# Kernel tuning notes

Hardware: AMD Instinct MI355X
Metric: run time of the kernel (lower is better)

## Reference

```python
import jax, jax.numpy as jnp
import numpy as np

EPS = 1e-5  # BatchNorm1d default eps


def _knn_idx(coords, k):
    # squared pairwise distances via gram trick (monotone in cdist, same topk order)
    sq = jnp.sum(coords * coords, axis=-1)                     # [B,N]
    d2 = sq[:, :, None] + sq[:, None, :] - 2.0 * jnp.einsum('bnd,bmd->bnm', coords, coords)
    _, idx = jax.lax.top_k(-d2, k)                             # smallest distances
    return idx                                                  # [B,N,k]


def _shared_mlp(x, W, b, gamma, beta):
    # Linear -> BatchNorm1d (training-mode batch stats over B,N per channel) -> ReLU
    y = x @ W + b                                              # [B,N,C]
    m = jnp.mean(y, axis=(0, 1))
    v = jnp.var(y, axis=(0, 1))                                # biased, as torch BN
    y = (y - m) / jnp.sqrt(v + EPS) * gamma + beta
    return jax.nn.relu(y)


def setup_inputs() -> dict:
    key = jax.random.key(0)
    ks = jax.random.split(key, 16)
    B, N, in_ch, out_ch, k = 4, 8192, 64, 128, 16
    mid = out_ch // 2
    s = 0.05
    inp = {
        'coords': jax.random.normal(ks[0], (B, N, 3), jnp.float32),
        'feats': jax.random.normal(ks[1], (B, N, in_ch), jnp.float32),
        'k': k,
        'W1': jax.random.normal(ks[2], (in_ch, mid), jnp.float32) * s,
        'b1': jnp.zeros((mid,), jnp.float32),
        'g1': jnp.ones((mid,), jnp.float32),
        'be1': jnp.zeros((mid,), jnp.float32),
        'Wa': jax.random.normal(ks[3], (mid, mid), jnp.float32) * s,
        'ba': jnp.zeros((mid,), jnp.float32),
        'ga': jnp.ones((mid,), jnp.float32),
        'bea': jnp.zeros((mid,), jnp.float32),
        'W2': jax.random.normal(ks[4], (mid, out_ch), jnp.float32) * s,
        'b2': jnp.zeros((out_ch,), jnp.float32),
        'g2': jnp.ones((out_ch,), jnp.float32),
        'be2': jnp.zeros((out_ch,), jnp.float32),
    }
    return inp


def reference(coords, feats, k, W1, b1, g1, be1, Wa, ba, ga, bea, W2, b2, g2, be2):
    B, N, _ = coords.shape
    idx = _knn_idx(coords, k)                                  # [B,N,k]
    # gather neighbor features: feats[b, idx[b,n,j]]
    neighbors = feats[jnp.arange(B)[:, None, None], idx]       # [B,N,k,C_in]
    agg = _shared_mlp(neighbors.mean(axis=2), W1, b1, g1, be1) # [B,N,mid]
    attn = jax.nn.sigmoid(_shared_mlp(agg, Wa, ba, ga, bea))
    fused = agg * attn + agg
    return _shared_mlp(fused, W2, b2, g2, be2)                 # [B,N,out_ch]
```

## Files before the change

### kernel.cpp

```cpp
#include <hip/hip_runtime.h>
#include <hip/hip_bf16.h>
#include <hip/hip_fp16.h>
#include <math.h>

#define B_ 4
#define N_ 8192
#define K_ 16
#define BN_ (B_ * N_)
#define EPS_ 1e-5f

#define S_ 8
#define TPB (S_ * 64)
#define QPB 64
#define MCAND (N_ / S_)
#define DEPTH 16

#define NBLK 512
#define ROWS 64

__global__ __launch_bounds__(256) void pack_coords(const float* __restrict__ coords,
                                                   float4* __restrict__ out) {
    int i = blockIdx.x * 256 + threadIdx.x;
    if (i >= BN_) return;
    out[i] = make_float4(coords[3 * i], coords[3 * i + 1], coords[3 * i + 2], 0.0f);
}

__global__ __launch_bounds__(256) void feats2h(const float* __restrict__ in,
                                               __half* __restrict__ outh) {
    int i = blockIdx.x * 256 + threadIdx.x;
    const float4* p = (const float4*)(in + (size_t)i * 8);
    float4 a = p[0], b = p[1];
    __half2 h0; h0.x = __float2half_rn(a.x); h0.y = __float2half_rn(a.y);
    __half2 h1; h1.x = __float2half_rn(a.z); h1.y = __float2half_rn(a.w);
    __half2 h2; h2.x = __float2half_rn(b.x); h2.y = __float2half_rn(b.y);
    __half2 h3; h3.x = __float2half_rn(b.z); h3.y = __float2half_rn(b.w);
    uint4 o;
    o.x = *(unsigned*)&h0; o.y = *(unsigned*)&h1; o.z = *(unsigned*)&h2; o.w = *(unsigned*)&h3;
    ((uint4*)outh)[i] = o;
}

__global__ __launch_bounds__(512) void knn_kernel(const float4* __restrict__ coords4,
                                                  int* __restrict__ idxOut) {
    __shared__ float2 bufp[DEPTH][TPB];
    __shared__ float thr2d[S_][64];

    const int bpb = N_ / QPB;
    int b = blockIdx.x / bpb;
    int qbase = (blockIdx.x % bpb) * QPB;
    int t = threadIdx.x;
    int lane = t & 63;
    int w = __builtin_amdgcn_readfirstlane(t >> 6);
    int q = qbase + lane;

    thr2d[t >> 6][lane] = 3.4e38f;
    __syncthreads();

    const float4* cb = coords4 + (size_t)b * N_;
    float4 qc = cb[q];
    float qx = qc.x, qy = qc.y, qz = qc.z;

    float key[K_];
    int   id[K_];
#pragma unroll
    for (int j = 0; j < K_; j++) { key[j] = 3.4e38f; id[j] = -1; }

    int cnt = 0;
    float bound = 3.4e38f;
    float lim = 3.4e38f;

    auto flush = [&]() {
        for (int j = 0; j < cnt; ++j) {
            float2 e = bufp[j][t];
            float d2 = e.x;
            int   m  = __float_as_int(e.y);
            if (d2 < key[K_ - 1]) {
#pragma unroll
                for (int jj = K_ - 1; jj > 0; --jj) {
                    bool up = d2 < key[jj - 1];
                    float ik = fminf(d2, key[jj]);
                    int   ii = (d2 < key[jj]) ? m : id[jj];
                    key[jj] = up ? key[jj - 1] : ik;
                    id[jj]  = up ? id[jj - 1]  : ii;
                }
                if (d2 < key[0]) { key[0] = d2; id[0] = m; }
            }
        }
        cnt = 0;
    };

    auto proc = [&](float4 c, int m) {
        float dx = qx - c.x, dy = qy - c.y, dz = qz - c.z;
        float d2 = dx * dx;
        d2 = fmaf(dy, dy, d2);
        d2 = fmaf(dz, dz, d2);
        if (d2 < lim) {
            bufp[cnt][t] = make_float2(d2, __int_as_float(m));
            cnt++;
        }
    };

    const int base = w * MCAND;
    for (int i = 0; i < MCAND; i += 8) {
        float4 c0 = cb[base + i + 0];
        float4 c1 = cb[base + i + 1];
        float4 c2 = cb[base + i + 2];
        float4 c3 = cb[base + i + 3];
        float4 c4 = cb[base + i + 4];
        float4 c5 = cb[base + i + 5];
        float4 c6 = cb[base + i + 6];
        float4 c7 = cb[base + i + 7];
        proc(c0, base + i + 0);
        proc(c1, base + i + 1);
        proc(c2, base + i + 2);
        proc(c3, base + i + 3);
        proc(c4, base + i + 4);
        proc(c5, base + i + 5);
        proc(c6, base + i + 6);
        proc(c7, base + i + 7);
        if (__any(cnt >= DEPTH - 7)) {
            flush();
            lim = fminf(key[K_ - 1], bound);
        }
        if ((i & 56) == 56) {
            thr2d[w][lane] = key[K_ - 1];
            float m0 = fminf(thr2d[0][lane], thr2d[1][lane]);
            float m1 = fminf(thr2d[2][lane], thr2d[3][lane]);
            float m2 = fminf(thr2d[4][lane], thr2d[5][lane]);
            float m3 = fminf(thr2d[6][lane], thr2d[7][lane]);
            bound = fminf(fminf(m0, m1), fminf(m2, m3));
            lim = fminf(key[K_ - 1], bound);
        }
    }
    flush();

#pragma unroll
    for (int j = 0; j < K_; j++) bufp[j][t] = make_float2(key[j], __int_as_float(id[j]));

    int* op = idxOut + ((size_t)b * N_ + q) * K_;
    for (int step = 1; step < S_; step <<= 1) {
        bool active = (w & (2 * step - 1)) == 0;
        float md[K_];
        int   mi[K_];
        __syncthreads();
        if (active) {
            int pa = t, pb = t + step * 64;
            int ia = 0, ib = 0;
#pragma unroll
            for (int r = 0; r < K_; ++r) {
                float2 ea = bufp[ia][pa];
                float2 eb = bufp[ib][pb];
                bool sel = ea.x <= eb.x;
                md[r] = sel ? ea.x : eb.x;
                mi[r] = __float_as_int(sel ? ea.y : eb.y);
                ia += sel ? 1 : 0;
                ib += sel ? 0 : 1;
            }
        }
        __syncthreads();
        if (active) {
            if (step == S_ / 2) {
#pragma unroll
                for (int r = 0; r < K_; ++r) op[r] = mi[r];
            } else {
#pragma unroll
                for (int r = 0; r < K_; ++r) bufp[r][t] = make_float2(md[r], __int_as_float(mi[r]));
            }
        }
    }
}

__global__ __launch_bounds__(512) void g1_kernel(const __half* __restrict__ fh,
                                                 const int* __restrict__ idx,
                                                 const float* __restrict__ W1,
                                                 const float* __restrict__ b1,
                                                 float* __restrict__ Y1,
                                                 float* __restrict__ part1) {
    __shared__ float buf[ROWS][65];
    int t = threadIdx.x;
    int rl = t & 63;
    int h2 = __builtin_amdgcn_readfirstlane(t >> 6);
    int vbid = ((blockIdx.x & 7) << 6) + (blockIdx.x >> 3);
    int row = vbid * ROWS + rl;
    int bb = row >> 13;

    const __half* fb = fh + ((size_t)bb << 13) * 64;
    const int* ip = idx + (size_t)row * K_;

    float xh[8];
#pragma unroll
    for (int j = 0; j < 8; j++) xh[j] = 0.0f;
#pragma unroll
    for (int j = 0; j < K_; j++) {
        uint4 a = *(const uint4*)(fb + (((size_t)ip[j]) << 6) + h2 * 8);
        __half2* hp = (__half2*)&a;
#pragma unroll
        for (int p = 0; p < 4; p++) {
            float2 f = __half22float2(hp[p]);
            xh[2 * p] += f.x;
            xh[2 * p + 1] += f.y;
        }
    }
#pragma unroll
    for (int j = 0; j < 8; j++) buf[rl][h2 * 8 + j] = xh[j] * (1.0f / 16.0f);
    __syncthreads();

    float acc[8];
#pragma unroll
    for (int j = 0; j < 8; j++) acc[j] = b1[h2 * 8 + j];
#pragma unroll 1
    for (int c0 = 0; c0 < 64; c0 += 16) {
        float xr[16];
#pragma unroll
        for (int j = 0; j < 16; j++) xr[j] = buf[rl][c0 + j];
#pragma unroll
        for (int cc = 0; cc < 16; cc++) {
            float xv = xr[cc];
            const float* wr = W1 + (c0 + cc) * 64 + h2 * 8;
#pragma unroll
            for (int j = 0; j < 8; j++) acc[j] = fmaf(xv, wr[j], acc[j]);
        }
    }
    float2* yp = (float2*)(Y1 + (size_t)row * 64 + h2 * 8);
#pragma unroll
    for (int f = 0; f < 4; f++) yp[f] = make_float2(acc[2 * f], acc[2 * f + 1]);
    __syncthreads();
#pragma unroll
    for (int j = 0; j < 8; j++) buf[rl][h2 * 8 + j] = acc[j];
    __syncthreads();
    if (t < 128) {
        int c = t & 63;
        float s = 0.0f;
        if (t < 64) { for (int r = 0; r < ROWS; ++r) s += buf[r][c]; }
        else        { for (int r = 0; r < ROWS; ++r) { float v = buf[r][c]; s = fmaf(v, v, s); } }
        part1[blockIdx.x * 128 + t] = s;
    }
}

__device__ __forceinline__ void reduce_stats64(const float* __restrict__ part,
                                               const float* __restrict__ gma,
                                               const float* __restrict__ bta,
                                               float* red4, float* scs, float* shs) {
    int t = threadIdx.x;
    {
        int c = t & 127;
        int q = t >> 7;
        float s = 0.0f;
#pragma unroll 8
        for (int g = q * 128; g < q * 128 + 128; ++g) s += part[(size_t)g * 128 + c];
        red4[t] = s;
    }
    __syncthreads();
    if (t < 128) red4[t] = red4[t] + red4[t + 128] + red4[t + 256] + red4[t + 384];
    __syncthreads();
    if (t < 64) {
        float mean = red4[t] * (1.0f / BN_);
        float var = red4[t + 64] * (1.0f / BN_) - mean * mean;
        float rstd = rsqrtf(var + EPS_);
        float scl = rstd * gma[t];
        scs[t] = scl;
        shs[t] = bta[t] - mean * scl;
    }
    __syncthreads();
}

__global__ __launch_bounds__(512) void m2_kernel(const float* __restrict__ Y1,
                                                 const float* __restrict__ Wa,
                                                 const float* __restrict__ ba,
                                                 const float* __restrict__ g1,
                                                 const float* __restrict__ be1,
                                                 const float* __restrict__ part1,
                                                 float* __restrict__ X1,
                                                 float* __restrict__ Y2,
                                                 float* __restrict__ part2) {
    __shared__ float buf[ROWS][65];
    __shared__ float red4[512];
    __shared__ float scs[64], shs[64];
    int t = threadIdx.x;
    int rl = t & 63;
    int h2 = __builtin_amdgcn_readfirstlane(t >> 6);
    int row = blockIdx.x * ROWS + rl;

    reduce_stats64(part1, g1, be1, red4, scs, shs);

    const float2* y1p = (const float2*)(Y1 + (size_t)row * 64 + h2 * 8);
    float2* x1p = (float2*)(X1 + (size_t)row * 64 + h2 * 8);
#pragma unroll
    for (int f = 0; f < 4; f++) {
        float2 v = y1p[f];
        int c0 = h2 * 8 + 2 * f;
        float a = fmaxf(0.0f, fmaf(v.x, scs[c0], shs[c0]));
        float b = fmaxf(0.0f, fmaf(v.y, scs[c0 + 1], shs[c0 + 1]));
        x1p[f] = make_float2(a, b);
        buf[rl][c0] = a;
        buf[rl][c0 + 1] = b;
    }
    __syncthreads();

    float acc[8];
#pragma unroll
    for (int j = 0; j < 8; j++) acc[j] = ba[h2 * 8 + j];
#pragma unroll 1
    for (int c0 = 0; c0 < 64; c0 += 16) {
        float xr[16];
#pragma unroll
        for (int j = 0; j < 16; j++) xr[j] = buf[rl][c0 + j];
#pragma unroll
        for (int cc = 0; cc < 16; cc++) {
            float xv = xr[cc];
            const float* wr = Wa + (c0 + cc) * 64 + h2 * 8;
#pragma unroll
            for (int j = 0; j < 8; j++) acc[j] = fmaf(xv, wr[j], acc[j]);
        }
    }
    float2* y2p = (float2*)(Y2 + (size_t)row * 64 + h2 * 8);
#pragma unroll
    for (int f = 0; f < 4; f++) y2p[f] = make_float2(acc[2 * f], acc[2 * f + 1]);
    __syncthreads();
#pragma unroll
    for (int j = 0; j < 8; j++) buf[rl][h2 * 8 + j] = acc[j];
    __syncthreads();
    if (t < 128) {
        int c = t & 63;
        float s = 0.0f;
        if (t < 64) { for (int r = 0; r < ROWS; ++r) s += buf[r][c]; }
        else        { for (int r = 0; r < ROWS; ++r) { float v = buf[r][c]; s = fmaf(v, v, s); } }
        part2[blockIdx.x * 128 + t] = s;
    }
}

__global__ __launch_bounds__(512) void m3_kernel(const float* __restrict__ Y2,
                                                 const float* __restrict__ X1,
                                                 const float* __restrict__ W2,
                                                 const float* __restrict__ b2,
                                                 const float* __restrict__ ga,
                                                 const float* __restrict__ bea,
                                                 const float* __restrict__ part2,
                                                 float* __restrict__ Y3,
                                                 float* __restrict__ part3) {
    __shared__ float buf[ROWS][65];
    __shared__ float red4[512];
    __shared__ float scs[64], shs[64];
    int t = threadIdx.x;
    int rl = t & 63;
    int h2 = __builtin_amdgcn_readfirstlane(t >> 6);
    int row = blockIdx.x * ROWS + rl;

    reduce_stats64(part2, ga, bea, red4, scs, shs);

    const float2* y2p = (const float2*)(Y2 + (size_t)row * 64 + h2 * 8);
    const float2* x1p = (const float2*)(X1 + (size_t)row * 64 + h2 * 8);
#pragma unroll
    for (int f = 0; f < 4; f++) {
        float2 v = y2p[f];
        float2 u = x1p[f];
        int c0 = h2 * 8 + 2 * f;
        float t0 = fmaxf(0.0f, fmaf(v.x, scs[c0], shs[c0]));
        float t1 = fmaxf(0.0f, fmaf(v.y, scs[c0 + 1], shs[c0 + 1]));
        float a0 = 1.0f / (1.0f + __expf(-t0));
        float a1 = 1.0f / (1.0f + __expf(-t1));
        buf[rl][c0] = u.x * (1.0f + a0);
        buf[rl][c0 + 1] = u.y * (1.0f + a1);
    }
    __syncthreads();

    float acc16[16];
#pragma unroll
    for (int j = 0; j < 16; j++) acc16[j] = b2[h2 * 16 + j];
#pragma unroll 1
    for (int c0 = 0; c0 < 64; c0 += 16) {
        float xr[16];
#pragma unroll
        for (int j = 0; j < 16; j++) xr[j] = buf[rl][c0 + j];
#pragma unroll
        for (int cc = 0; cc < 16; cc++) {
            float xv = xr[cc];
            const float* wr = W2 + (c0 + cc) * 128 + h2 * 16;
#pragma unroll
            for (int j = 0; j < 16; j++) acc16[j] = fmaf(xv, wr[j], acc16[j]);
        }
    }
    float4* yp = (float4*)(Y3 + (size_t)row * 128 + h2 * 16);
#pragma unroll
    for (int f = 0; f < 4; f++)
        yp[f] = make_float4(acc16[4 * f], acc16[4 * f + 1], acc16[4 * f + 2], acc16[4 * f + 3]);

    __syncthreads();
    if (h2 < 4) {
#pragma unroll
        for (int j = 0; j < 16; j++) buf[rl][h2 * 16 + j] = acc16[j];
    }
    __syncthreads();
    if (t < 128) {
        int c = t & 63;
        float s = 0.0f;
        if (t < 64) { for (int r = 0; r < ROWS; ++r) s += buf[r][c]; }
        else        { for (int r = 0; r < ROWS; ++r) { float v = buf[r][c]; s = fmaf(v, v, s); } }
        part3[blockIdx.x * 256 + t] = s;
    }
    __syncthreads();
    if (h2 >= 4) {
#pragma unroll
        for (int j = 0; j < 16; j++) buf[rl][(h2 - 4) * 16 + j] = acc16[j];
    }
    __syncthreads();
    if (t < 128) {
        int c = t & 63;
        float s = 0.0f;
        if (t < 64) { for (int r = 0; r < ROWS; ++r) s += buf[r][c]; }
        else        { for (int r = 0; r < ROWS; ++r) { float v = buf[r][c]; s = fmaf(v, v, s); } }
        part3[blockIdx.x * 256 + 128 + t] = s;
    }
}

__global__ __launch_bounds__(256) void bnf_kernel(float* __restrict__ Y3,
                                                  const float* __restrict__ g2,
                                                  const float* __restrict__ be2,
                                                  const float* __restrict__ part3) {
    __shared__ float red[256];
    __shared__ float scs[128], shs[128];
    int t = threadIdx.x;
    {
        float s = 0.0f;
#pragma unroll 8
        for (int g = 0; g < NBLK; ++g) s += part3[(size_t)g * 256 + t];
        red[t] = s;
    }
    __syncthreads();
    if (t < 128) {
        int si = (t < 64) ? t : (t + 64);
        float mean = red[si] * (1.0f / BN_);
        float var = red[si + 64] * (1.0f / BN_) - mean * mean;
        float rstd = rsqrtf(var + EPS_);
        float scl = rstd * g2[t];
        scs[t] = scl;
        shs[t] = be2[t] - mean * scl;
    }
    __syncthreads();
    const int total = BN_ * 128 / 4;
    float4* p = (float4*)Y3;
    for (int i = blockIdx.x * 256 + t; i < total; i += 256 * 256) {
        float4 v = p[i];
        int c0 = (i * 4) & 127;
        v.x = fmaxf(0.0f, fmaf(v.x, scs[c0],     shs[c0]));
        v.y = fmaxf(0.0f, fmaf(v.y, scs[c0 + 1], shs[c0 + 1]));
        v.z = fmaxf(0.0f, fmaf(v.z, scs[c0 + 2], shs[c0 + 2]));
        v.w = fmaxf(0.0f, fmaf(v.w, scs[c0 + 3], shs[c0 + 3]));
        p[i] = v;
    }
}

extern "C" void kernel_launch(void* const* d_in, const int* in_sizes, int n_in,
                              void* d_out, int out_size, void* d_ws, size_t ws_size,
                              hipStream_t stream) {
    const float* coords = (const float*)d_in[0];
    const float* feats  = (const float*)d_in[1];
    const float* W1  = (const float*)d_in[3];
    const float* b1  = (const float*)d_in[4];
    const float* g1  = (const float*)d_in[5];
    const float* be1 = (const float*)d_in[6];
    const float* Wa  = (const float*)d_in[7];
    const float* ba  = (const float*)d_in[8];
    const float* ga  = (const float*)d_in[9];
    const float* bea = (const float*)d_in[10];
    const float* W2  = (const float*)d_in[11];
    const float* b2  = (const float*)d_in[12];
    const float* g2  = (const float*)d_in[13];
    const float* be2 = (const float*)d_in[14];

    float* ws = (float*)d_ws;
    float4* coords4 = (float4*)ws;
    int*    idxbuf  = (int*)(ws + 131072);
    __half* fh      = (__half*)(ws + 131072 + 524288);
    float*  y1 = ws + 131072 + 524288 + 1048576;
    float*  x1 = y1 + (size_t)BN_ * 64;
    float*  y2 = x1 + (size_t)BN_ * 64;
    float*  part1 = y2 + (size_t)BN_ * 64;
    float*  part2 = part1 + NBLK * 128;
    float*  part3 = part2 + NBLK * 128;
    float*  y3 = (float*)d_out;

    pack_coords<<<(BN_ + 255) / 256, 256, 0, stream>>>(coords, coords4);
    feats2h<<<BN_ * 64 / 8 / 256, 256, 0, stream>>>(feats, fh);
    knn_kernel<<<B_ * (N_ / QPB), TPB, 0, stream>>>(coords4, idxbuf);

    g1_kernel<<<NBLK, 512, 0, stream>>>(fh, idxbuf, W1, b1, y1, part1);
    m2_kernel<<<NBLK, 512, 0, stream>>>(y1, Wa, ba, g1, be1, part1, x1, y2, part2);
    m3_kernel<<<NBLK, 512, 0, stream>>>(y2, x1, W2, b2, ga, bea, part2, y3, part3);
    bnf_kernel<<<256, 256, 0, stream>>>(y3, g2, be2, part3);
}
```

Before: 287.2 us.

## Replace KNN adaptive bound sharing with two-pass exponent histogram threshold

The KNN kernel now makes a first pass over all candidates to build a per-query histogram of squared-distance exponents in shared memory. From it, it derives a conservative threshold that is guaranteed to admit at least K candidates, then runs a second filtered insertion pass using packed 64-bit (distance,index) keys. This removes the cross-wave bound exchange and halves the register sort work, aiming to filter far more candidates early. The cost is a second full scan of the coordinates and per-candidate shared-memory histogram increments.

```diff
diff --git a/kernel.cpp b/kernel.cpp
--- a/kernel.cpp
+++ b/kernel.cpp
@@ -9,14 +9,15 @@
 #define BN_ (B_ * N_)
 #define EPS_ 1e-5f
 
-#define S_ 8
-#define TPB (S_ * 64)
-#define QPB 64
-#define MCAND (N_ / S_)
+#define KW_ 8
+#define KT_ (KW_ * 64)
+#define MCAND (N_ / KW_)
 #define DEPTH 16
 
 #define NBLK 512
 #define ROWS 64
+
+#define KEY_SENTINEL 0x7F800000FFFFFFFFULL
 
 __global__ __launch_bounds__(256) void pack_coords(const float* __restrict__ coords,
                                                    float4* __restrict__ out) {
@@ -39,67 +40,30 @@
     ((uint4*)outh)[i] = o;
 }
 
-__global__ __launch_bounds__(512) void knn_kernel(const float4* __restrict__ coords4,
-                                                  int* __restrict__ idxOut) {
-    __shared__ float2 bufp[DEPTH][TPB];
-    __shared__ float thr2d[S_][64];
-
-    const int bpb = N_ / QPB;
-    int b = blockIdx.x / bpb;
-    int qbase = (blockIdx.x % bpb) * QPB;
+__global__ __launch_bounds__(KT_) void knn_hist(const float4* __restrict__ coords4,
+                                                int* __restrict__ idxOut) {
+    __shared__ unsigned long long bufp[DEPTH][KT_];
+    __shared__ unsigned short hist[KW_][16][64];
+
     int t = threadIdx.x;
     int lane = t & 63;
     int w = __builtin_amdgcn_readfirstlane(t >> 6);
-    int q = qbase + lane;
-
-    thr2d[t >> 6][lane] = 3.4e38f;
-    __syncthreads();
+    int b = blockIdx.x >> 7;
+    int g = blockIdx.x & 127;
+
+    {
+        unsigned* hp = (unsigned*)hist;
+        for (int i = t; i < KW_ * 16 * 64 / 2; i += KT_) hp[i] = 0;
+    }
 
     const float4* cb = coords4 + (size_t)b * N_;
+    int q = g * 64 + lane;
     float4 qc = cb[q];
     float qx = qc.x, qy = qc.y, qz = qc.z;
-
-    float key[K_];
-    int   id[K_];
-#pragma unroll
-    for (int j = 0; j < K_; j++) { key[j] = 3.4e38f; id[j] = -1; }
-
-    int cnt = 0;
-    float bound = 3.4e38f;
-    float lim = 3.4e38f;
-
-    auto flush = [&]() {
-        for (int j = 0; j < cnt; ++j) {
-            float2 e = bufp[j][t];
-            float d2 = e.x;
-            int   m  = __float_as_int(e.y);
-            if (d2 < key[K_ - 1]) {
-#pragma unroll
-                for (int jj = K_ - 1; jj > 0; --jj) {
-                    bool up = d2 < key[jj - 1];
-                    float ik = fminf(d2, key[jj]);
-                    int   ii = (d2 < key[jj]) ? m : id[jj];
-                    key[jj] = up ? key[jj - 1] : ik;
-                    id[jj]  = up ? id[jj - 1]  : ii;
-                }
-                if (d2 < key[0]) { key[0] = d2; id[0] = m; }
-            }
-        }
-        cnt = 0;
-    };
-
-    auto proc = [&](float4 c, int m) {
-        float dx = qx - c.x, dy = qy - c.y, dz = qz - c.z;
-        float d2 = dx * dx;
-        d2 = fmaf(dy, dy, d2);
-        d2 = fmaf(dz, dz, d2);
-        if (d2 < lim) {
-            bufp[cnt][t] = make_float2(d2, __int_as_float(m));
-            cnt++;
-        }
-    };
+    __syncthreads();
 
     const int base = w * MCAND;
+
     for (int i = 0; i < MCAND; i += 8) {
         float4 c0 = cb[base + i + 0];
         float4 c1 = cb[base + i + 1];
@@ -109,61 +73,118 @@
         float4 c5 = cb[base + i + 5];
         float4 c6 = cb[base + i + 6];
         float4 c7 = cb[base + i + 7];
-        proc(c0, base + i + 0);
-        proc(c1, base + i + 1);
-        proc(c2, base + i + 2);
-        proc(c3, base + i + 3);
-        proc(c4, base + i + 4);
-        proc(c5, base + i + 5);
-        proc(c6, base + i + 6);
-        proc(c7, base + i + 7);
-        if (__any(cnt >= DEPTH - 7)) {
-            flush();
-            lim = fminf(key[K_ - 1], bound);
-        }
-        if ((i & 56) == 56) {
-            thr2d[w][lane] = key[K_ - 1];
-            float m0 = fminf(thr2d[0][lane], thr2d[1][lane]);
-            float m1 = fminf(thr2d[2][lane], thr2d[3][lane]);
-            float m2 = fminf(thr2d[4][lane], thr2d[5][lane]);
-            float m3 = fminf(thr2d[6][lane], thr2d[7][lane]);
-            bound = fminf(fminf(m0, m1), fminf(m2, m3));
-            lim = fminf(key[K_ - 1], bound);
-        }
+#define H1(cv)                                                         \
+        {                                                              \
+            float dx = qx - cv.x, dy = qy - cv.y, dz = qz - cv.z;      \
+            float d2 = dx * dx;                                        \
+            d2 = fmaf(dy, dy, d2);                                     \
+            d2 = fmaf(dz, dz, d2);                                     \
+            int e = (int)(__float_as_uint(d2) >> 23);                  \
+            int bk = e - 117;                                          \
+            bk = bk < 0 ? 0 : (bk > 15 ? 15 : bk);                     \
+            hist[w][bk][lane] = (unsigned short)(hist[w][bk][lane] + 1); \
+        }
+        H1(c0) H1(c1) H1(c2) H1(c3) H1(c4) H1(c5) H1(c6) H1(c7)
+#undef H1
+    }
+    __syncthreads();
+
+    float T;
+    {
+        int cum = 0;
+        int B = 16;
+        for (int bb = 0; bb < 16; ++bb) {
+            int c = 0;
+#pragma unroll
+            for (int ww = 0; ww < KW_; ++ww) c += hist[ww][bb][lane];
+            cum += c;
+            if (cum >= K_ && B == 16) B = bb;
+        }
+        T = (B >= 15) ? 3.4e38f : __uint_as_float((unsigned)(118 + B) << 23);
+    }
+
+    unsigned long long key[K_];
+#pragma unroll
+    for (int j = 0; j < K_; j++) key[j] = KEY_SENTINEL;
+
+    int cnt = 0;
+    float limf = T;
+
+    auto flush = [&]() {
+        for (int j = 0; j < cnt; ++j) {
+            unsigned long long e = bufp[j][t];
+            if (e < key[K_ - 1]) {
+#pragma unroll
+                for (int jj = K_ - 1; jj > 0; --jj) {
+                    bool up = e < key[jj - 1];
+                    unsigned long long lo = (e < key[jj]) ? e : key[jj];
+                    key[jj] = up ? key[jj - 1] : lo;
+                }
+                if (e < key[0]) key[0] = e;
+            }
+        }
+        cnt = 0;
+        float own = __uint_as_float((unsigned)(key[K_ - 1] >> 32));
+        limf = fminf(own, T);
+    };
+
+    for (int i = 0; i < MCAND; i += 8) {
+        float4 c0 = cb[base + i + 0];
+        float4 c1 = cb[base + i + 1];
+        float4 c2 = cb[base + i + 2];
+        float4 c3 = cb[base + i + 3];
+        float4 c4 = cb[base + i + 4];
+        float4 c5 = cb[base + i + 5];
+        float4 c6 = cb[base + i + 6];
+        float4 c7 = cb[base + i + 7];
+#define P2(cv, mm)                                                     \
+        {                                                              \
+            float dx = qx - cv.x, dy = qy - cv.y, dz = qz - cv.z;      \
+            float d2 = dx * dx;                                        \
+            d2 = fmaf(dy, dy, d2);                                     \
+            d2 = fmaf(dz, dz, d2);                                     \
+            if (d2 < limf) {                                           \
+                bufp[cnt][t] = ((unsigned long long)__float_as_uint(d2) << 32) | \
+                               (unsigned)(mm);                         \
+                cnt++;                                                 \
+            }                                                          \
+        }
+        P2(c0, base + i + 0) P2(c1, base + i + 1) P2(c2, base + i + 2) P2(c3, base + i + 3)
+        P2(c4, base + i + 4) P2(c5, base + i + 5) P2(c6, base + i + 6) P2(c7, base + i + 7)
+#undef P2
+        if (__any(cnt >= DEPTH - 7)) flush();
     }
     flush();
 
 #pragma unroll
-    for (int j = 0; j < K_; j++) bufp[j][t] = make_float2(key[j], __int_as_float(id[j]));
+    for (int j = 0; j < K_; j++) bufp[j][t] = key[j];
 
     int* op = idxOut + ((size_t)b * N_ + q) * K_;
-    for (int step = 1; step < S_; step <<= 1) {
+    for (int step = 1; step < KW_; step <<= 1) {
         bool active = (w & (2 * step - 1)) == 0;
-        float md[K_];
-        int   mi[K_];
+        unsigned long long md[K_];
         __syncthreads();
         if (active) {
             int pa = t, pb = t + step * 64;
             int ia = 0, ib = 0;
 #pragma unroll
-            for (int r = 0; r < K_; ++r) {
-                float2 ea = bufp[ia][pa];
-                float2 eb = bufp[ib][pb];
-                bool sel = ea.x <= eb.x;
-                md[r] = sel ? ea.x : eb.x;
-                mi[r] = __float_as_int(sel ? ea.y : eb.y);
+            for (int r2 = 0; r2 < K_; ++r2) {
+                unsigned long long ea = bufp[ia][pa];
+                unsigned long long eb = bufp[ib][pb];
+                bool sel = ea <= eb;
+                md[r2] = sel ? ea : eb;
                 ia += sel ? 1 : 0;
                 ib += sel ? 0 : 1;
             }
         }
         __syncthreads();
         if (active) {
-            if (step == S_ / 2) {
-#pragma unroll
-                for (int r = 0; r < K_; ++r) op[r] = mi[r];
+            if (step == KW_ / 2) {
+#pragma unroll
+                for (int r2 = 0; r2 < K_; ++r2) op[r2] = (int)(md[r2] & 0xFFFFFFFFu);
             } else {
 #pragma unroll
-                for (int r = 0; r < K_; ++r) bufp[r][t] = make_float2(md[r], __int_as_float(mi[r]));
+                for (int r2 = 0; r2 < K_; ++r2) bufp[r2][t] = md[r2];
             }
         }
     }
@@ -481,7 +502,7 @@
 
     pack_coords<<<(BN_ + 255) / 256, 256, 0, stream>>>(coords, coords4);
     feats2h<<<BN_ * 64 / 8 / 256, 256, 0, stream>>>(feats, fh);
-    knn_kernel<<<B_ * (N_ / QPB), TPB, 0, stream>>>(coords4, idxbuf);
+    knn_hist<<<B_ * 128, KT_, 0, stream>>>(coords4, idxbuf);
 
     g1_kernel<<<NBLK, 512, 0, stream>>>(fh, idxbuf, W1, b1, y1, part1);
     m2_kernel<<<NBLK, 512, 0, stream>>>(y1, Wa, ba, g1, be1, part1, x1, y2, part2);
```

Result: faster. 273.4 us (-4.8%).
